# Kernel tuning notes

Hardware: AMD Instinct MI355X
Metric: run time of the kernel (lower is better)

Reference implementation:

```python
import jax, jax.numpy as jnp
import numpy as np

# norse LIFParameters defaults with method='super', alpha=100
TAU_SYN_INV = 200.0
TAU_MEM_INV = 100.0
V_LEAK = 0.0
V_TH = 1.0
V_RESET = 0.0
ALPHA = 100.0
DT = 0.001
SEQ_LENGTH = 100

@jax.custom_vjp
def super_spike(x):
    return (x > 0).astype(x.dtype)

def _ss_fwd(x):
    return super_spike(x), x

def _ss_bwd(x, g):
    # SuperSpike surrogate: dz/dx = 1 / (alpha*|x| + 1)^2
    return (g / (ALPHA * jnp.abs(x) + 1.0) ** 2,)

super_spike.defvjp(_ss_fwd, _ss_bwd)

def lif_step(inp, v, i):
    v_dec = v + DT * TAU_MEM_INV * ((V_LEAK - v) + i)
    i_dec = i * (1.0 - DT * TAU_SYN_INV)
    z = super_spike(v_dec - V_TH)
    v_new = (1.0 - z) * v_dec + z * V_RESET
    i_new = i_dec + inp
    return z, v_new, i_new

def setup_inputs() -> dict:
    key = jax.random.key(0)
    ks = jax.random.split(key, 5)
    B, F, H, C = 16384, 256, 256, 10
    x = jax.random.normal(ks[0], (B, F), dtype=jnp.float32)
    W_hidden = jax.random.normal(ks[1], (H, F), dtype=jnp.float32) / np.sqrt(F)
    b_hidden = jax.random.normal(ks[2], (H,), dtype=jnp.float32) * 0.01
    W_readout = jax.random.normal(ks[3], (C, H), dtype=jnp.float32) / np.sqrt(H)
    b_readout = jax.random.normal(ks[4], (C,), dtype=jnp.float32) * 0.01
    return {"x": x, "W_hidden": W_hidden, "b_hidden": b_hidden,
            "W_readout": W_readout, "b_readout": b_readout}

def reference(x, W_hidden, b_hidden, W_readout, b_readout):
    B, F = x.shape
    H = W_hidden.shape[0]
    z0 = jnp.zeros((B, F), x.dtype)
    z1 = jnp.zeros((B, H), x.dtype)

    def step(carry, _):
        v1, i1, v2, i2, acc = carry
        # input LIF cell (same input current x at every timestep)
        z, v1, i1 = lif_step(x, v1, i1)
        h = jnp.einsum('bf,hf->bh', z, W_hidden) + b_hidden
        # output LIF cell
        z2, v2, i2 = lif_step(h, v2, i2)
        return (v1, i1, v2, i2, acc + z2), None

    carry0 = (z0, z0, z1, z1, z1)
    (v1, i1, v2, i2, acc), _ = jax.lax.scan(step, carry0, None, length=SEQ_LENGTH)
    mean_spikes = acc / SEQ_LENGTH  # == outputs.mean(0)
    return jnp.einsum('bh,ch->bc', mean_spikes, W_readout) + b_readout
```

## Files before the change

### kernel.cpp

```cpp
#include <hip/hip_runtime.h>
#include <hip/hip_fp16.h>
#include <stdint.h>


#define BB 16384
#define FF 256
#define HH 256
#define CC 10
#define TT 100

typedef __attribute__((ext_vector_type(4))) int int4v;

__global__ __launch_bounds__(256) void spike_gen(
    const float* __restrict__ x, unsigned long long* __restrict__ Z) {
  const int lane = threadIdx.x & 63;
  const int wv   = threadIdx.x >> 6;
  const int b0   = blockIdx.x * 8 + wv * 2;
  const float K_VM = (float)(0.001 * 100.0);
  const float K_ID = (float)(1.0 - 0.001 * 200.0);

  float v[8], cur[8], xv[8];
#pragma unroll
  for (int jb = 0; jb < 2; ++jb)
#pragma unroll
    for (int js = 0; js < 4; ++js) {
      const int idx = jb * 4 + js;
      xv[idx] = x[(size_t)(b0 + jb) * FF + js * 64 + lane];
      v[idx] = 0.0f; cur[idx] = 0.0f;
    }

  const bool s0 = (lane & 1) != 0, s1 = (lane & 2) != 0, s2 = (lane & 4) != 0;
  unsigned long long* zp = Z + (size_t)b0 * 4;

  for (int t4 = 0; t4 < TT; t4 += 4) {
    unsigned long long mq[4];
#pragma unroll
    for (int k = 0; k < 4; ++k) {
      unsigned long long bal[8];
#pragma unroll
      for (int idx = 0; idx < 8; ++idx) {
        float vd   = __fadd_rn(v[idx], __fmul_rn(K_VM, __fadd_rn(-v[idx], cur[idx])));
        float idec = __fmul_rn(cur[idx], K_ID);
        bool z = (vd > 1.0f);
        bal[idx] = __ballot(z);
        v[idx]   = z ? 0.0f : vd;
        cur[idx] = __fadd_rn(idec, xv[idx]);
      }
      unsigned long long m0 = s0 ? bal[1] : bal[0];
      unsigned long long m1 = s0 ? bal[3] : bal[2];
      unsigned long long m2 = s0 ? bal[5] : bal[4];
      unsigned long long m3 = s0 ? bal[7] : bal[6];
      unsigned long long n0 = s1 ? m1 : m0;
      unsigned long long n1 = s1 ? m3 : m2;
      mq[k] = s2 ? n1 : n0;
    }
    if (lane < 8) {
#pragma unroll
      for (int k = 0; k < 4; ++k)
        zp[(size_t)(t4 + k) * (BB * 4) + lane] = mq[k];
    }
  }
}

__global__ __launch_bounds__(256, 4) void snn_main(
    const uint32_t* __restrict__ Z, const float* __restrict__ Wh,
    const float* __restrict__ bh, const float* __restrict__ Wr,
    const float* __restrict__ br, float* __restrict__ out) {
  __shared__ __align__(16) char WS[32768];

  const int tid = threadIdx.x;
  const int bx  = blockIdx.x;
  const int hc  = bx & 3;
  const int bc  = bx >> 2;
  const int h0  = hc * 64;
  const int b0  = bc * 64;

  {
    int4v* ws4 = (int4v*)WS;
#pragma unroll
    for (int half = 0; half < 4; ++half) {
      const int u  = tid + half * 256;
      const int rr = u >> 4;
      const int q  = u & 15;
      const int s  = q >> 2, kq = q & 3;
      const int nt = rr >> 4, n = rr & 15;
      const float* wp = Wh + (size_t)(h0 + rr) * FF + s * 64 + kq * 16;
      uint32_t pa[4], pb[4];
#pragma unroll
      for (int c4 = 0; c4 < 4; ++c4) {
        float4 w4 = *(const float4*)(wp + c4 * 4);
        float wf[4] = {w4.x, w4.y, w4.z, w4.w};
        uint32_t ua = 0, ub = 0;
#pragma unroll
        for (int e = 0; e < 4; ++e) {
          float af = rintf(wf[e] * 256.0f);
          af = fminf(fmaxf(af, -127.0f), 127.0f);
          float bf = rintf(__builtin_fmaf(af, -64.0f, wf[e] * 16384.0f));
          bf = fminf(fmaxf(bf, -127.0f), 127.0f);
          ua |= ((uint32_t)((int)af) & 255u) << (8 * e);
          ub |= ((uint32_t)((int)bf) & 255u) << (8 * e);
        }
        pa[c4] = ua; pb[c4] = ub;
      }
      ws4[((nt * 2 + 0) * 4 + s) * 64 + kq * 16 + n] = *(int4v*)pa;
      ws4[((nt * 2 + 1) * 4 + s) * 64 + kq * 16 + n] = *(int4v*)pb;
    }
  }
  __syncthreads();

  const int lane = tid & 63;
  const int bsub = tid >> 6;
  const int col  = lane & 15;
  const int quad = lane >> 4;
  const bool qhi = (quad & 2) != 0;
  const uint32_t shl16 = (quad & 1) * 16;

  const int brow = b0 + bsub * 16 + col;

  const float K_VM = (float)(0.001 * 100.0);
  const float K_ID = (float)(1.0 - 0.001 * 200.0);

  float v2[4][4], ii[4][4];
  uint32_t sc[4];
#pragma unroll
  for (int nt = 0; nt < 4; ++nt) {
    sc[nt] = 0u;
#pragma unroll
    for (int r = 0; r < 4; ++r) { v2[nt][r] = 0.f; ii[nt][r] = 0.f; }
  }

  float bias[4];
#pragma unroll
  for (int nt = 0; nt < 4; ++nt) bias[nt] = bh[h0 + nt * 16 + col];

  uint32_t hw0[2], hw1[2], hw2[2], hw3[2];
  const uint32_t* zrow = Z + (size_t)brow * 8;

  auto load_plane = [&](int t, int j) {
    const uint32_t* p = zrow + (size_t)t * (size_t)(BB * 8);
    uint4 a = *(const uint4*)p;
    uint4 b4 = *(const uint4*)(p + 4);
    hw0[j] = (qhi ? a.y : a.x) >> shl16;
    hw1[j] = (qhi ? a.w : a.z) >> shl16;
    hw2[j] = (qhi ? b4.y : b4.x) >> shl16;
    hw3[j] = (qhi ? b4.w : b4.z) >> shl16;
  };

  const char* wsl = WS + lane * 16;
  int4v acc[2][4];

  auto kloop2 = [&]() {
#pragma unroll
    for (int j = 0; j < 2; ++j)
#pragma unroll
      for (int nt = 0; nt < 4; ++nt)
        acc[j][nt] = (int4v){0, 0, 0, 0};
#pragma unroll 1
    for (int s = 0; s < 4; ++s) {
      const int4v* bp = (const int4v*)(wsl + s * 1024);
      int4v Ba[4], Bb[4];
#pragma unroll
      for (int nt = 0; nt < 4; ++nt) {
        Ba[nt] = bp[(nt * 2 + 0) * 256];
        Bb[nt] = bp[(nt * 2 + 1) * 256];
      }
#pragma unroll
      for (int j = 0; j < 2; ++j) {
        uint32_t t0 = (s & 1) ? hw1[j] : hw0[j];
        uint32_t t1 = (s & 1) ? hw3[j] : hw2[j];
        uint32_t h16 = (s & 2) ? t1 : t0;
        int4v za, zb_;
#pragma unroll
        for (int p = 0; p < 4; ++p) {
          uint32_t nib = (h16 >> (4 * p)) & 15u;
          uint32_t zbyte = __umul24(nib, 0x204081u) & 0x01010101u;
          zb_[p] = (int)zbyte;
          za[p]  = (int)(zbyte << 6);
        }
#pragma unroll
        for (int nt = 0; nt < 4; ++nt) {
          acc[j][nt] = __builtin_amdgcn_mfma_i32_16x16x64_i8(
              za, Ba[nt], acc[j][nt], 0, 0, 0);
          acc[j][nt] = __builtin_amdgcn_mfma_i32_16x16x64_i8(
              zb_, Bb[nt], acc[j][nt], 0, 0, 0);
        }
      }
    }
  };

  auto lifp = [&](int j) {
#pragma unroll
    for (int nt = 0; nt < 4; ++nt) {
#pragma unroll
      for (int r = 0; r < 4; ++r) {
        float h  = __builtin_fmaf((float)acc[j][nt][r], 6.103515625e-05f,
                                  bias[nt]);
        float vv = v2[nt][r], ci = ii[nt][r];
        float vd   = __fadd_rn(vv, __fmul_rn(K_VM, __fadd_rn(-vv, ci)));
        float idec = __fmul_rn(ci, K_ID);
        bool z = (vd > 1.0f);
        v2[nt][r] = z ? 0.0f : vd;
        ii[nt][r] = __fadd_rn(idec, h);
        sc[nt] += (z ? 1u : 0u) << (8 * r);
      }
    }
  };

  const int stag = ((bx >> 5) ^ (bx >> 8)) & 1;

  if (stag) {
    load_plane(0, 0); load_plane(0, 1);
    kloop2();
    load_plane(1, 0); load_plane(2, 1);
    lifp(0);
#pragma unroll 1
    for (int k = 0; k < 49; ++k) {
      kloop2();
      if (k < 48) { load_plane(3 + 2 * k, 0); load_plane(4 + 2 * k, 1); }
      else        { load_plane(99, 0);         load_plane(99, 1); }
      lifp(0); lifp(1);
    }
    kloop2();
    lifp(0);
  } else {
    load_plane(0, 0); load_plane(1, 1);
#pragma unroll 1
    for (int k = 0; k < 50; ++k) {
      kloop2();
      if (k < 49) { load_plane(2 + 2 * k, 0); load_plane(3 + 2 * k, 1); }
      lifp(0); lifp(1);
    }
  }

  float mean[4][4];
#pragma unroll
  for (int nt = 0; nt < 4; ++nt)
#pragma unroll
    for (int r = 0; r < 4; ++r)
      mean[nt][r] = __fdiv_rn((float)((sc[nt] >> (8 * r)) & 255u), 100.0f);

#pragma unroll 1
  for (int c = 0; c < CC; ++c) {
    float wc[4];
#pragma unroll
    for (int nt = 0; nt < 4; ++nt) wc[nt] = Wr[c * HH + h0 + nt * 16 + col];
#pragma unroll
    for (int r = 0; r < 4; ++r) {
      float s = 0.f;
#pragma unroll
      for (int nt = 0; nt < 4; ++nt) s = fmaf(mean[nt][r], wc[nt], s);
      s += __shfl_xor(s, 1);
      s += __shfl_xor(s, 2);
      s += __shfl_xor(s, 4);
      s += __shfl_xor(s, 8);
      if (col == 0) {
        int b = b0 + bsub * 16 + quad * 4 + r;
        float add = s + ((hc == 0) ? br[c] : 0.0f);
        atomicAdd(&out[b * CC + c], add);
      }
    }
  }
}

extern "C" void kernel_launch(void* const* d_in, const int* in_sizes, int n_in,
                              void* d_out, int out_size, void* d_ws, size_t ws_size,
                              hipStream_t stream) {
  const float* x  = (const float*)d_in[0];
  const float* Wh = (const float*)d_in[1];
  const float* bh = (const float*)d_in[2];
  const float* Wr = (const float*)d_in[3];
  const float* br = (const float*)d_in[4];
  float* out = (float*)d_out;

  unsigned long long* Z = (unsigned long long*)d_ws;

  hipMemsetAsync(d_out, 0, (size_t)out_size * sizeof(float), stream);
  spike_gen<<<BB / 8, 256, 0, stream>>>(x, Z);
  snn_main<<<1024, 256, 0, stream>>>((const uint32_t*)Z, Wh, bh, Wr, br, out);
}
```

Measured before the change: 396.1 us.

## Double-buffer MFMA accumulators to overlap LIF update with next timestep matmul

Replaces the staggered single-accumulator loop with two accumulator sets (accA/accB), so the MFMA work for the next pair of timesteps is issued before the LIF update of the previous pair. This lets matrix-core work overlap with the VALU-heavy LIF math and hides the accumulator dependency. It removes the block-parity stagger scheme and doubles accumulator register use, which risks spills or lower occupancy under launch_bounds(256,4).

```diff
diff --git a/kernel.cpp b/kernel.cpp
--- a/kernel.cpp
+++ b/kernel.cpp
@@ -136,20 +136,23 @@
   uint32_t hw0[2], hw1[2], hw2[2], hw3[2];
   const uint32_t* zrow = Z + (size_t)brow * 8;
 
-  auto load_plane = [&](int t, int j) {
-    const uint32_t* p = zrow + (size_t)t * (size_t)(BB * 8);
-    uint4 a = *(const uint4*)p;
-    uint4 b4 = *(const uint4*)(p + 4);
-    hw0[j] = (qhi ? a.y : a.x) >> shl16;
-    hw1[j] = (qhi ? a.w : a.z) >> shl16;
-    hw2[j] = (qhi ? b4.y : b4.x) >> shl16;
-    hw3[j] = (qhi ? b4.w : b4.z) >> shl16;
+  auto load_hw = [&](int tgi) {
+#pragma unroll
+    for (int j = 0; j < 2; ++j) {
+      const uint32_t* p = zrow + ((size_t)tgi * 2 + j) * (size_t)(BB * 8);
+      uint4 a = *(const uint4*)p;
+      uint4 b4 = *(const uint4*)(p + 4);
+      hw0[j] = (qhi ? a.y : a.x) >> shl16;
+      hw1[j] = (qhi ? a.w : a.z) >> shl16;
+      hw2[j] = (qhi ? b4.y : b4.x) >> shl16;
+      hw3[j] = (qhi ? b4.w : b4.z) >> shl16;
+    }
   };
 
   const char* wsl = WS + lane * 16;
-  int4v acc[2][4];
-
-  auto kloop2 = [&]() {
+  int4v accA[2][4], accB[2][4];
+
+  auto kloop2 = [&](int4v (&acc)[2][4]) {
 #pragma unroll
     for (int j = 0; j < 2; ++j)
 #pragma unroll
@@ -188,49 +191,42 @@
     }
   };
 
-  auto lifp = [&](int j) {
-#pragma unroll
-    for (int nt = 0; nt < 4; ++nt) {
-#pragma unroll
-      for (int r = 0; r < 4; ++r) {
-        float h  = __builtin_fmaf((float)acc[j][nt][r], 6.103515625e-05f,
-                                  bias[nt]);
-        float vv = v2[nt][r], ci = ii[nt][r];
-        float vd   = __fadd_rn(vv, __fmul_rn(K_VM, __fadd_rn(-vv, ci)));
-        float idec = __fmul_rn(ci, K_ID);
-        bool z = (vd > 1.0f);
-        v2[nt][r] = z ? 0.0f : vd;
-        ii[nt][r] = __fadd_rn(idec, h);
-        sc[nt] += (z ? 1u : 0u) << (8 * r);
+  auto lif2 = [&](int4v (&acc)[2][4]) {
+#pragma unroll
+    for (int j = 0; j < 2; ++j) {
+#pragma unroll
+      for (int nt = 0; nt < 4; ++nt) {
+#pragma unroll
+        for (int r = 0; r < 4; ++r) {
+          float h  = __builtin_fmaf((float)acc[j][nt][r], 6.103515625e-05f,
+                                    bias[nt]);
+          float vv = v2[nt][r], ci = ii[nt][r];
+          float vd   = __fadd_rn(vv, __fmul_rn(K_VM, __fadd_rn(-vv, ci)));
+          float idec = __fmul_rn(ci, K_ID);
+          bool z = (vd > 1.0f);
+          v2[nt][r] = z ? 0.0f : vd;
+          ii[nt][r] = __fadd_rn(idec, h);
+          sc[nt] += (z ? 1u : 0u) << (8 * r);
+        }
       }
     }
   };
 
-  const int stag = ((bx >> 5) ^ (bx >> 8)) & 1;
-
-  if (stag) {
-    load_plane(0, 0); load_plane(0, 1);
-    kloop2();
-    load_plane(1, 0); load_plane(2, 1);
-    lifp(0);
+  load_hw(0);
+  kloop2(accA);
+  load_hw(1);
 #pragma unroll 1
-    for (int k = 0; k < 49; ++k) {
-      kloop2();
-      if (k < 48) { load_plane(3 + 2 * k, 0); load_plane(4 + 2 * k, 1); }
-      else        { load_plane(99, 0);         load_plane(99, 1); }
-      lifp(0); lifp(1);
-    }
-    kloop2();
-    lifp(0);
-  } else {
-    load_plane(0, 0); load_plane(1, 1);
-#pragma unroll 1
-    for (int k = 0; k < 50; ++k) {
-      kloop2();
-      if (k < 49) { load_plane(2 + 2 * k, 0); load_plane(3 + 2 * k, 1); }
-      lifp(0); lifp(1);
-    }
-  }
+  for (int it = 0; it < 24; ++it) {
+    kloop2(accB);
+    load_hw(2 * it + 2);
+    lif2(accA);
+    kloop2(accA);
+    load_hw(2 * it + 3);
+    lif2(accB);
+  }
+  kloop2(accB);
+  lif2(accA);
+  lif2(accB);
 
   float mean[4][4];
 #pragma unroll
```

New measurement: 774.3 us. 1.95x slower.
